# Optimization experiments

Measured on AMD Instinct MI355X. Metric: run time of the kernel, lower is better.

## Reference

```python
import jax, jax.numpy as jnp
import numpy as np

NUM_CLASSES = 20
FC = 512  # feature_channels
H = W = 28


def _conv(x, w, b):
    y = jax.lax.conv_general_dilated(x, w, (1, 1), 'SAME',
                                     dimension_numbers=('NCHW', 'OIHW', 'NCHW'))
    return y + b[None, :, None, None]


def _center_map(centers, height, width):
    # centers: [B, N, 4] = (x, y, class, conf); vectorized scatter replacing the python loop
    B, N, _ = centers.shape
    xp = (centers[..., 0] * width).astype(jnp.int32)   # int() truncation; x>=0 so == floor
    yp = (centers[..., 1] * height).astype(jnp.int32)
    conf = centers[..., 3]
    valid = (xp >= 0) & (xp < width) & (yp >= 0) & (yp < height)
    flat = jnp.where(valid, yp * width + xp, height * width)  # invalid -> dummy slot
    m = jnp.zeros((B, height * width + 1), centers.dtype)
    m = m.at[jnp.arange(B)[:, None], flat].set(conf)
    return m[:, :height * width].reshape(B, 1, height, width)


def setup_inputs() -> dict:
    key = jax.random.key(0)
    ks = jax.random.split(key, 16)
    B = 256
    image = jax.random.normal(ks[0], (B, 3, H, W), jnp.float32)
    features = jax.random.normal(ks[1], (B, FC, 7, 7), jnp.float32)
    centers = jax.random.uniform(ks[2], (B, 100, 4), jnp.float32)

    def conv_w(k, co, ci):
        s = 1.0 / np.sqrt(ci * 9)
        return jax.random.uniform(k, (co, ci, 3, 3), jnp.float32, -s, s)

    def lin_w(k, co, ci):
        s = 1.0 / np.sqrt(ci)
        return jax.random.uniform(k, (co, ci), jnp.float32, -s, s)

    cin = FC + 3 + 1  # 516
    return {
        'image': image, 'features': features, 'centers': centers,
        'w1': conv_w(ks[3], 128, cin), 'b1': jnp.zeros((128,), jnp.float32),
        'w2': conv_w(ks[4], 64, 128), 'b2': jnp.zeros((64,), jnp.float32),
        'w3': conv_w(ks[5], 32, 64), 'b3': jnp.zeros((32,), jnp.float32),
        'w4': conv_w(ks[6], 16, 32), 'b4': jnp.zeros((16,), jnp.float32),
        'fw1': lin_w(ks[7], 256, 16 * H * W), 'fb1': jnp.zeros((256,), jnp.float32),
        'fw2': lin_w(ks[8], 4 + NUM_CLASSES, 256), 'fb2': jnp.zeros((4 + NUM_CLASSES,), jnp.float32),
    }


def reference(image, features, centers, w1, b1, w2, b2, w3, b3, w4, b4, fw1, fb1, fw2, fb2):
    B = image.shape[0]
    feats = jax.image.resize(features, (B, FC, H, W), method='bilinear')  # align_corners=False
    cmap = _center_map(centers, H, W)
    x = jnp.concatenate([image, feats, cmap], axis=1)  # [B, 516, 28, 28]
    x = jax.nn.relu(_conv(x, w1, b1))
    x = jax.nn.relu(_conv(x, w2, b2))
    x = jax.nn.relu(_conv(x, w3, b3))
    x = jax.nn.relu(_conv(x, w4, b4))
    x = x.reshape(B, -1)
    x = jax.nn.relu(x @ fw1.T + fb1)
    action = x @ fw2.T + fb2  # [B, 4 + num_classes]
    action = action.at[:, 2].set(jax.nn.sigmoid(action[:, 2]))
    action = action.at[:, 3].set(jax.nn.sigmoid(action[:, 3]))
    return action
```

## Files before the change

kernel.cpp:

```cpp
#include <hip/hip_runtime.h>

typedef _Float16 f16;
typedef _Float16 f16x8 __attribute__((ext_vector_type(8)));
typedef float    f32x4 __attribute__((ext_vector_type(4)));

static __device__ __forceinline__ f16x8 ld8(const f16* p) {
    return *reinterpret_cast<const f16x8*>(p);
}

static constexpr size_t W1T_B  = 1253376;
static constexpr size_t W2T_B  = 147456;
static constexpr size_t W3T_B  = 36864;
static constexpr size_t W4T_B  = 9216;
static constexpr size_t FW1T_B = 6422528;
static constexpr size_t WEIGHTS_B = W1T_B + W2T_B + W3T_B + W4T_B + FW1T_B;

static constexpr size_t PB_X0 = 979200;
static constexpr size_t PB_X1 = 230400;
static constexpr size_t PB_X2 = 115200;
static constexpr size_t PB_X3 = 57600;
static constexpr size_t PB_X4 = 25088;
static constexpr size_t PB_X5 = 512;
static constexpr size_t PER_BATCH = PB_X0 + PB_X1 + PB_X2 + PB_X3 + PB_X4 + PB_X5;

static __device__ __forceinline__ void wxf(const float* __restrict__ w, f16* __restrict__ wt,
                                           int i, int CINr, int NCB, int COUT) {
    int co = i % COUT;
    int r  = i / COUT;
    int hi = r & 3; r >>= 2;
    int cb = r % NCB;
    int tap = r / NCB;
    f16x8 v;
    #pragma unroll
    for (int j = 0; j < 8; ++j) {
        int ci = cb * 32 + hi * 8 + j;
        float x = (ci < CINr) ? w[((size_t)co * CINr + ci) * 9 + tap] : 0.f;
        v[j] = (f16)x;
    }
    *reinterpret_cast<f16x8*>(wt + (size_t)i * 8) = v;
}

static constexpr int S1 = 9 * 17 * 4 * 128;
static constexpr int S2 = 9 * 4  * 4 * 64;
static constexpr int S3 = 9 * 2  * 4 * 32;
static constexpr int S4 = 9 * 1  * 4 * 16;
static constexpr int SW = S1 + S2 + S3 + S4;
static constexpr int SFW = 256 * 12544;
static constexpr int PREP_TOT = SW + SFW;

__global__ void prep_all(const float* __restrict__ w1, const float* __restrict__ w2,
                         const float* __restrict__ w3, const float* __restrict__ w4,
                         const float* __restrict__ fw1,
                         f16* __restrict__ W1t, f16* __restrict__ W2t,
                         f16* __restrict__ W3t, f16* __restrict__ W4t,
                         f16* __restrict__ FW1t) {
    int t = blockIdx.x * 256 + threadIdx.x;
    if (t >= PREP_TOT) return;
    if (t < S1) { wxf(w1, W1t, t, 516, 17, 128); return; }
    t -= S1;
    if (t < S2) { wxf(w2, W2t, t, 128, 4, 64); return; }
    t -= S2;
    if (t < S3) { wxf(w3, W3t, t, 64, 2, 32); return; }
    t -= S3;
    if (t < S4) { wxf(w4, W4t, t, 32, 1, 16); return; }
    t -= S4;
    int o = t / 12544, idx = t % 12544;
    int y = idx / 448, rem = idx % 448;
    int x = rem / 16, c = rem & 15;
    FW1t[t] = (f16)fw1[(size_t)o * 12544 + c * 784 + y * 28 + x];
}

static __device__ __forceinline__ void ring_yx(int bi, int& y, int& x) {
    if (bi < 30)      { y = 0;        x = bi; }
    else if (bi < 60) { y = 29;       x = bi - 30; }
    else if (bi < 88) { y = bi - 59;  x = 0; }
    else              { y = bi - 87;  x = 29; }
}

__global__ __launch_bounds__(512) void build_x0(
        const float* __restrict__ img, const float* __restrict__ feat,
        const float* __restrict__ centers,
        f16* __restrict__ X0, f16* __restrict__ X1,
        f16* __restrict__ X2, f16* __restrict__ X3, int b0) {
    const int bl = blockIdx.x;
    const int b  = b0 + bl;
    const int tid = threadIdx.x;
    f16* x0b = X0 + (size_t)bl * (17 * 900 * 32);

    for (int i = tid; i < 116 * 544; i += 512) {
        int c = i % 544, bi = i / 544;
        int y, x; ring_yx(bi, y, x);
        x0b[((size_t)(c >> 5) * 900 + y * 30 + x) * 32 + (c & 31)] = (f16)0.f;
    }
    for (int i = tid; i < 784; i += 512) {
        int y = i / 28, x = i % 28;
        x0b[((size_t)16 * 900 + (y + 1) * 30 + x + 1) * 32 + 3] = (f16)0.f;
    }
    for (int i = tid; i < 3 * 784; i += 512) {
        int c = i / 784, p = i % 784;
        int y = p / 28, x = p % 28;
        x0b[((size_t)(y + 1) * 30 + x + 1) * 32 + c] =
            (f16)img[((size_t)b * 3 + c) * 784 + p];
    }
    {
        const int c  = tid + 3;
        const int cb = c >> 5, c32 = c & 31;
        const float* fb = feat + ((size_t)b * 512 + tid) * 49;
        float r0[7], r1[7];
        int cur = -100;
        for (int y = 0; y < 28; ++y) {
            float sy = (y + 0.5f) * 0.25f - 0.5f;
            float fy = floorf(sy);
            int iy0 = (int)fy;
            float wy1 = sy - fy, wy0 = 1.f - wy1;
            if (iy0 != cur) {
                cur = iy0;
                int i0 = iy0 < 0 ? 0 : iy0;
                int i1 = (iy0 + 1 > 6) ? 6 : iy0 + 1;
                #pragma unroll
                for (int j = 0; j < 7; ++j) { r0[j] = fb[i0 * 7 + j]; r1[j] = fb[i1 * 7 + j]; }
            }
            f16* orow = x0b + ((size_t)cb * 900 + (y + 1) * 30 + 1) * 32 + c32;
            #pragma unroll 28
            for (int x = 0; x < 28; ++x) {
                float sx = (x + 0.5f) * 0.25f - 0.5f;
                float fx = floorf(sx);
                int ix0 = (int)fx;
                float wx1 = sx - fx, wx0 = 1.f - wx1;
                int j0 = ix0 < 0 ? 0 : ix0;
                int j1 = (ix0 + 1 > 6) ? 6 : ix0 + 1;
                float v = wy0 * (wx0 * r0[j0] + wx1 * r0[j1]) +
                          wy1 * (wx0 * r1[j0] + wx1 * r1[j1]);
                orow[(size_t)x * 32] = (f16)v;
            }
        }
    }
    {
        f16* x1b = X1 + (size_t)bl * (4 * 900 * 32);
        for (int i = tid; i < 116 * 128; i += 512) {
            int c = i % 128, bi = i / 128;
            int y, x; ring_yx(bi, y, x);
            x1b[((size_t)(c >> 5) * 900 + y * 30 + x) * 32 + (c & 31)] = (f16)0.f;
        }
        f16* x2b = X2 + (size_t)bl * (2 * 900 * 32);
        for (int i = tid; i < 116 * 64; i += 512) {
            int c = i % 64, bi = i / 64;
            int y, x; ring_yx(bi, y, x);
            x2b[((size_t)(c >> 5) * 900 + y * 30 + x) * 32 + (c & 31)] = (f16)0.f;
        }
        f16* x3b = X3 + (size_t)bl * (900 * 32);
        for (int i = tid; i < 116 * 32; i += 512) {
            int c = i % 32, bi = i / 32;
            int y, x; ring_yx(bi, y, x);
            x3b[((size_t)y * 30 + x) * 32 + c] = (f16)0.f;
        }
    }
    __syncthreads();
    if (tid == 0) {
        const float* cb = centers + (size_t)b * 400;
        for (int n = 0; n < 100; ++n) {
            float cx = cb[n * 4 + 0], cy = cb[n * 4 + 1], conf = cb[n * 4 + 3];
            int xp = (int)(cx * 28.f);
            int yp = (int)(cy * 28.f);
            if (xp >= 0 && xp < 28 && yp >= 0 && yp < 28)
                x0b[((size_t)16 * 900 + (yp + 1) * 30 + xp + 1) * 32 + 3] = (f16)conf;
        }
    }
}

template<int CIN, int COUT, int GM, int GN, int WNT, int MW, bool PADOUT, int RGR>
__global__ __launch_bounds__(512) void conv3x3(const f16* __restrict__ Xin,
                                               const f16* __restrict__ Wt,
                                               const float* __restrict__ bias,
                                               f16* __restrict__ Xout) {
    constexpr int NCB  = CIN / 32;
    constexpr int NCBO = COUT / 32;
    constexpr int NV_B = 9 * 4 * COUT;
    constexpr int PT   = (NV_B + 511) / 512;
    __shared__ f16 Bs[NV_B * 8];

    const int rg = blockIdx.x;
    const int b  = blockIdx.y;
    const int tid = threadIdx.x;
    const int wave = tid >> 6;
    const int lane = tid & 63;
    const int lm = lane & 15, hi = lane >> 4;
    const int wm = wave % GM, wn = wave / GM;
    const int rows = (28 - rg * RGR < RGR) ? (28 - rg * RGR) : RGR;
    const int MT = rows * 28 / 16;

    f32x4 acc[MW][WNT];
    #pragma unroll
    for (int k = 0; k < MW; ++k)
        #pragma unroll
        for (int n = 0; n < WNT; ++n)
            acc[k][n] = (f32x4){0.f, 0.f, 0.f, 0.f};

    const size_t bbase = (size_t)b * NCB * 900;
    int inoff[MW];
    #pragma unroll
    for (int k = 0; k < MW; ++k) {
        const int m = wm + k * GM;
        const int p = m * 16 + lm;
        const int yl = p / 28, x = p - yl * 28;
        inoff[k] = (m < MT) ? ((rg * RGR + yl) * 30 + x) : 0;
    }

    for (int cb = 0; cb < NCB; ++cb) {
        #pragma unroll
        for (int pi = 0; pi < PT; ++pi) {
            const int v = tid + pi * 512;
            if (v < NV_B) {
                const int tap = v / (4 * COUT);
                const int w   = v - tap * (4 * COUT);
                const f16* gsrc = Wt + ((size_t)(tap * NCB + cb) * (4 * COUT) + w) * 8;
                f16* ldst = Bs + (size_t)(pi * 512 + (tid & ~63)) * 8;
                __builtin_amdgcn_global_load_lds(
                    (const __attribute__((address_space(1))) void*)gsrc,
                    (__attribute__((address_space(3))) void*)ldst, 16, 0, 0);
            }
        }
        __syncthreads();

        #pragma unroll
        for (int tap = 0; tap < 9; ++tap) {
            f16x8 bf[WNT];
            #pragma unroll
            for (int n = 0; n < WNT; ++n)
                bf[n] = *reinterpret_cast<const f16x8*>(
                    Bs + ((size_t)(tap * 4 + hi) * COUT + (wn * WNT + n) * 16 + lm) * 8);
            const int dy = tap / 3, dx = tap - dy * 3;
            const size_t dOff = (bbase + (size_t)cb * 900 + dy * 30 + dx) * 32 + hi * 8;
            #pragma unroll
            for (int k = 0; k < MW; ++k) {
                if (wm + k * GM < MT) {
                    const f16x8 af = ld8(Xin + dOff + (size_t)inoff[k] * 32);
                    #pragma unroll
                    for (int n = 0; n < WNT; ++n)
                        acc[k][n] = __builtin_amdgcn_mfma_f32_16x16x32_f16(af, bf[n], acc[k][n], 0, 0, 0);
                }
            }
        }
        __syncthreads();
    }

    #pragma unroll
    for (int k = 0; k < MW; ++k) {
        const int m = wm + k * GM;
        if (m < MT) {
            #pragma unroll
            for (int n = 0; n < WNT; ++n) {
                const int co = (wn * WNT + n) * 16 + lm;
                const float bv = bias[co];
                #pragma unroll
                for (int r = 0; r < 4; ++r) {
                    const int p = m * 16 + hi * 4 + r;
                    const int yl = p / 28, x = p - yl * 28;
                    const float v = fmaxf(acc[k][n][r] + bv, 0.f);
                    size_t off;
                    if (PADOUT)
                        off = (((size_t)b * NCBO + (co >> 5)) * 900 +
                               (rg * RGR + yl + 1) * 30 + (x + 1)) * 32 + (co & 31);
                    else
                        off = ((size_t)b * 784 + (rg * RGR + yl) * 28 + x) * COUT + co;
                    Xout[off] = (f16)v;
                }
            }
        }
    }
}

__global__ __launch_bounds__(256) void fc1k(const f16* __restrict__ X4,
                                            const f16* __restrict__ FW1t,
                                            const float* __restrict__ fb1,
                                            f16* __restrict__ X5, int CH) {
    const int bm = blockIdx.x;
    const int nt = blockIdx.y * 4 + (threadIdx.x >> 6);
    const int lane = threadIdx.x & 63;
    const int lm = lane & 15, hi = lane >> 4;
    f32x4 acc = (f32x4){0.f, 0.f, 0.f, 0.f};
    const int row0 = bm * 16 + lm;
    const int rowA = (row0 < CH) ? row0 : 0;
    const f16* arow = X4 + (size_t)rowA * 12544;
    const int o = nt * 16 + lm;
    const f16* brow = FW1t + (size_t)o * 12544;
    for (int kk = 0; kk < 12544; kk += 32) {
        const f16x8 af = ld8(arow + kk + hi * 8);
        const f16x8 bf = ld8(brow + kk + hi * 8);
        acc = __builtin_amdgcn_mfma_f32_16x16x32_f16(af, bf, acc, 0, 0, 0);
    }
    const float bv = fb1[o];
    #pragma unroll
    for (int r = 0; r < 4; ++r) {
        const int row = bm * 16 + hi * 4 + r;
        if (row < CH)
            X5[(size_t)row * 256 + o] = (f16)fmaxf(acc[r] + bv, 0.f);
    }
}

__global__ void fc2k(const f16* __restrict__ X5, const float* __restrict__ fw2,
                     const float* __restrict__ fb2, float* __restrict__ out, int CH) {
    int t = blockIdx.x * 256 + threadIdx.x;
    if (t < CH * 24) {
        int b = t / 24, o = t % 24;
        float s = fb2[o];
        const f16* xr = X5 + (size_t)b * 256;
        const float* wr = fw2 + (size_t)o * 256;
        for (int k = 0; k < 256; ++k) s += (float)xr[k] * wr[k];
        if (o == 2 || o == 3) s = 1.f / (1.f + expf(-s));
        out[t] = s;
    }
}

extern "C" void kernel_launch(void* const* d_in, const int* in_sizes, int n_in,
                              void* d_out, int out_size, void* d_ws, size_t ws_size,
                              hipStream_t stream) {
    const float* image    = (const float*)d_in[0];
    const float* features = (const float*)d_in[1];
    const float* centers  = (const float*)d_in[2];
    const float* w1  = (const float*)d_in[3];
    const float* b1  = (const float*)d_in[4];
    const float* w2  = (const float*)d_in[5];
    const float* b2  = (const float*)d_in[6];
    const float* w3  = (const float*)d_in[7];
    const float* b3  = (const float*)d_in[8];
    const float* w4  = (const float*)d_in[9];
    const float* b4  = (const float*)d_in[10];
    const float* fw1 = (const float*)d_in[11];
    const float* fb1 = (const float*)d_in[12];
    const float* fw2 = (const float*)d_in[13];
    const float* fb2 = (const float*)d_in[14];

    int CH = 8;
    for (int c = 256; c >= 8; c >>= 1) {
        if (WEIGHTS_B + (size_t)c * PER_BATCH <= ws_size) { CH = c; break; }
    }

    char* ws = (char*)d_ws;
    f16* W1t  = (f16*)(ws);
    f16* W2t  = (f16*)(ws + W1T_B);
    f16* W3t  = (f16*)(ws + W1T_B + W2T_B);
    f16* W4t  = (f16*)(ws + W1T_B + W2T_B + W3T_B);
    f16* FW1t = (f16*)(ws + W1T_B + W2T_B + W3T_B + W4T_B);
    char* act = ws + WEIGHTS_B;
    f16* X0 = (f16*)(act);
    f16* X1 = (f16*)(act + (size_t)CH * PB_X0);
    f16* X2 = (f16*)(act + (size_t)CH * (PB_X0 + PB_X1));
    f16* X3 = (f16*)(act + (size_t)CH * (PB_X0 + PB_X1 + PB_X2));
    f16* X4 = (f16*)(act + (size_t)CH * (PB_X0 + PB_X1 + PB_X2 + PB_X3));
    f16* X5 = (f16*)(act + (size_t)CH * (PB_X0 + PB_X1 + PB_X2 + PB_X3 + PB_X4));

    prep_all<<<(PREP_TOT + 255) / 256, 256, 0, stream>>>(w1, w2, w3, w4, fw1,
                                                         W1t, W2t, W3t, W4t, FW1t);

    for (int b0 = 0; b0 < 256; b0 += CH) {
        build_x0<<<CH, 512, 0, stream>>>(image, features, centers,
                                         X0, X1, X2, X3, b0);

        conv3x3<544, 128, 4, 2, 4, 2, true, 4><<<dim3(7, CH), 512, 0, stream>>>(X0, W1t, b1, X1);
        dim3 cgrid(4, CH);
        conv3x3<128, 64,  4, 2, 2, 4, true, 8><<<cgrid, 512, 0, stream>>>(X1, W2t, b2, X2);
        conv3x3<64,  32,  4, 2, 1, 4, true, 8><<<cgrid, 512, 0, stream>>>(X2, W3t, b3, X3);
        conv3x3<32,  16,  8, 1, 1, 2, false, 8><<<cgrid, 512, 0, stream>>>(X3, W4t, b4, X4);

        dim3 fgrid((CH + 15) / 16, 4);
        fc1k<<<fgrid, 256, 0, stream>>>(X4, FW1t, fb1, X5, CH);
        fc2k<<<(CH * 24 + 255) / 256, 256, 0, stream>>>(X5, fw2, fb2,
                                                        (float*)d_out + (size_t)b0 * 24, CH);
    }
}
```

Baseline: 917.6 us.

## Split conv1 input channels across two blocks and fuse bias+ReLU in a reduction pass

The first 3x3 conv (544->128 channels) now splits its input-channel loop into two halves along a new grid z dimension. Each half writes raw fp16 partial sums to its own buffer, and a new sum_relu kernel adds the two partials, applies bias and ReLU, and writes into the padded X1 layout. The row-group height also doubles from 4 to 8 rows per block, with more M tiles per wave, so each weight chunk staged in LDS is reused over more output pixels. The intent is to cut per-block weight staging and keep enough blocks in flight. The cost is an extra activation buffer, an extra kernel launch with a read-modify-write pass, and fp16 rounding of the partial sums before they are added.

```diff
diff --git a/kernel.cpp b/kernel.cpp
--- a/kernel.cpp
+++ b/kernel.cpp
@@ -15,13 +15,15 @@
 static constexpr size_t FW1T_B = 6422528;
 static constexpr size_t WEIGHTS_B = W1T_B + W2T_B + W3T_B + W4T_B + FW1T_B;
 
-static constexpr size_t PB_X0 = 979200;
-static constexpr size_t PB_X1 = 230400;
-static constexpr size_t PB_X2 = 115200;
-static constexpr size_t PB_X3 = 57600;
-static constexpr size_t PB_X4 = 25088;
-static constexpr size_t PB_X5 = 512;
-static constexpr size_t PER_BATCH = PB_X0 + PB_X1 + PB_X2 + PB_X3 + PB_X4 + PB_X5;
+static constexpr size_t PB_X0  = 979200;
+static constexpr size_t PB_X1  = 230400;
+static constexpr size_t PB_X1B = 230400;
+static constexpr size_t PB_X2  = 115200;
+static constexpr size_t PB_X3  = 57600;
+static constexpr size_t PB_X4  = 25088;
+static constexpr size_t PB_X5  = 512;
+static constexpr size_t PER_BATCH =
+    PB_X0 + PB_X1 + PB_X1B + PB_X2 + PB_X3 + PB_X4 + PB_X5;
 
 static __device__ __forceinline__ void wxf(const float* __restrict__ w, f16* __restrict__ wt,
                                            int i, int CINr, int NCB, int COUT) {
@@ -168,19 +170,23 @@
     }
 }
 
-template<int CIN, int COUT, int GM, int GN, int WNT, int MW, bool PADOUT, int RGR>
+template<int CIN, int COUT, int GM, int GN, int WNT, int MW, bool PADOUT, int RGR, int KS>
 __global__ __launch_bounds__(512) void conv3x3(const f16* __restrict__ Xin,
                                                const f16* __restrict__ Wt,
                                                const float* __restrict__ bias,
-                                               f16* __restrict__ Xout) {
+                                               f16* __restrict__ Xout, size_t zoff) {
     constexpr int NCB  = CIN / 32;
     constexpr int NCBO = COUT / 32;
     constexpr int NV_B = 9 * 4 * COUT;
     constexpr int PT   = (NV_B + 511) / 512;
+    constexpr int HALF = (NCB + KS - 1) / KS;
     __shared__ f16 Bs[NV_B * 8];
 
     const int rg = blockIdx.x;
     const int b  = blockIdx.y;
+    const int bz = (KS > 1) ? (int)blockIdx.z : 0;
+    const int cbA = bz * HALF;
+    const int cbB = (cbA + HALF < NCB) ? cbA + HALF : NCB;
     const int tid = threadIdx.x;
     const int wave = tid >> 6;
     const int lane = tid & 63;
@@ -206,7 +212,7 @@
         inoff[k] = (m < MT) ? ((rg * RGR + yl) * 30 + x) : 0;
     }
 
-    for (int cb = 0; cb < NCB; ++cb) {
+    for (int cb = cbA; cb < cbB; ++cb) {
         #pragma unroll
         for (int pi = 0; pi < PT; ++pi) {
             const int v = tid + pi * 512;
@@ -244,6 +250,7 @@
         __syncthreads();
     }
 
+    f16* xout = Xout + (size_t)bz * zoff;
     #pragma unroll
     for (int k = 0; k < MW; ++k) {
         const int m = wm + k * GM;
@@ -251,23 +258,46 @@
             #pragma unroll
             for (int n = 0; n < WNT; ++n) {
                 const int co = (wn * WNT + n) * 16 + lm;
-                const float bv = bias[co];
+                const float bv = (KS > 1) ? 0.f : bias[co];
                 #pragma unroll
                 for (int r = 0; r < 4; ++r) {
                     const int p = m * 16 + hi * 4 + r;
                     const int yl = p / 28, x = p - yl * 28;
-                    const float v = fmaxf(acc[k][n][r] + bv, 0.f);
+                    const float v = (KS > 1) ? acc[k][n][r]
+                                             : fmaxf(acc[k][n][r] + bv, 0.f);
                     size_t off;
                     if (PADOUT)
                         off = (((size_t)b * NCBO + (co >> 5)) * 900 +
                                (rg * RGR + yl + 1) * 30 + (x + 1)) * 32 + (co & 31);
                     else
                         off = ((size_t)b * 784 + (rg * RGR + yl) * 28 + x) * COUT + co;
-                    Xout[off] = (f16)v;
+                    xout[off] = (f16)v;
                 }
             }
         }
     }
+}
+
+__global__ void sum_relu(f16* __restrict__ X1a, const f16* __restrict__ X1b,
+                         const float* __restrict__ b1, int CH) {
+    int t = blockIdx.x * 256 + threadIdx.x;
+    const int tot = CH * 12544;
+    if (t >= tot) return;
+    int bl = t / 12544, r = t % 12544;
+    int ck = r / 3136, r2 = r % 3136;
+    int y = r2 / 112, w = r2 % 112;
+    int x = w >> 2, h = w & 3;
+    size_t base = (((size_t)bl * 4 + ck) * 900 + (y + 1) * 30 + (x + 1)) * 32 + h * 8;
+    f16x8 a = ld8(X1a + base);
+    f16x8 bb = ld8(X1b + base);
+    const float* bp = b1 + ck * 32 + h * 8;
+    f16x8 o;
+    #pragma unroll
+    for (int j = 0; j < 8; ++j) {
+        float s = (float)a[j] + (float)bb[j] + bp[j];
+        o[j] = (f16)fmaxf(s, 0.f);
+    }
+    *reinterpret_cast<f16x8*>(X1a + base) = o;
 }
 
 __global__ __launch_bounds__(256) void fc1k(const f16* __restrict__ X4,
@@ -343,25 +373,30 @@
     f16* W4t  = (f16*)(ws + W1T_B + W2T_B + W3T_B);
     f16* FW1t = (f16*)(ws + W1T_B + W2T_B + W3T_B + W4T_B);
     char* act = ws + WEIGHTS_B;
-    f16* X0 = (f16*)(act);
-    f16* X1 = (f16*)(act + (size_t)CH * PB_X0);
-    f16* X2 = (f16*)(act + (size_t)CH * (PB_X0 + PB_X1));
-    f16* X3 = (f16*)(act + (size_t)CH * (PB_X0 + PB_X1 + PB_X2));
-    f16* X4 = (f16*)(act + (size_t)CH * (PB_X0 + PB_X1 + PB_X2 + PB_X3));
-    f16* X5 = (f16*)(act + (size_t)CH * (PB_X0 + PB_X1 + PB_X2 + PB_X3 + PB_X4));
+    f16* X0  = (f16*)(act);
+    f16* X1a = (f16*)(act + (size_t)CH * PB_X0);
+    f16* X1b = (f16*)(act + (size_t)CH * (PB_X0 + PB_X1));
+    f16* X2  = (f16*)(act + (size_t)CH * (PB_X0 + PB_X1 + PB_X1B));
+    f16* X3  = (f16*)(act + (size_t)CH * (PB_X0 + PB_X1 + PB_X1B + PB_X2));
+    f16* X4  = (f16*)(act + (size_t)CH * (PB_X0 + PB_X1 + PB_X1B + PB_X2 + PB_X3));
+    f16* X5  = (f16*)(act + (size_t)CH * (PB_X0 + PB_X1 + PB_X1B + PB_X2 + PB_X3 + PB_X4));
+    const size_t zoffElems = (size_t)CH * (PB_X1 / 2);
 
     prep_all<<<(PREP_TOT + 255) / 256, 256, 0, stream>>>(w1, w2, w3, w4, fw1,
                                                          W1t, W2t, W3t, W4t, FW1t);
 
     for (int b0 = 0; b0 < 256; b0 += CH) {
         build_x0<<<CH, 512, 0, stream>>>(image, features, centers,
-                                         X0, X1, X2, X3, b0);
-
-        conv3x3<544, 128, 4, 2, 4, 2, true, 4><<<dim3(7, CH), 512, 0, stream>>>(X0, W1t, b1, X1);
+                                         X0, X1a, X2, X3, b0);
+
+        conv3x3<544, 128, 4, 2, 4, 4, true, 8, 2>
+            <<<dim3(4, CH, 2), 512, 0, stream>>>(X0, W1t, b1, X1a, zoffElems);
+        sum_relu<<<(CH * 12544 + 255) / 256, 256, 0, stream>>>(X1a, X1b, b1, CH);
+
         dim3 cgrid(4, CH);
-        conv3x3<128, 64,  4, 2, 2, 4, true, 8><<<cgrid, 512, 0, stream>>>(X1, W2t, b2, X2);
-        conv3x3<64,  32,  4, 2, 1, 4, true, 8><<<cgrid, 512, 0, stream>>>(X2, W3t, b3, X3);
-        conv3x3<32,  16,  8, 1, 1, 2, false, 8><<<cgrid, 512, 0, stream>>>(X3, W4t, b4, X4);
+        conv3x3<128, 64,  4, 2, 2, 4, true, 8, 1><<<cgrid, 512, 0, stream>>>(X1a, W2t, b2, X2, 0);
+        conv3x3<64,  32,  4, 2, 1, 4, true, 8, 1><<<cgrid, 512, 0, stream>>>(X2, W3t, b3, X3, 0);
+        conv3x3<32,  16,  8, 1, 1, 2, false, 8, 1><<<cgrid, 512, 0, stream>>>(X3, W4t, b4, X4, 0);
 
         dim3 fgrid((CH + 15) / 16, 4);
         fc1k<<<fgrid, 256, 0, stream>>>(X4, FW1t, fb1, X5, CH);
```

After: 913.4 us. About the same (-0.5%).
